# Kernel optimization log

Hardware: AMD Instinct MI355X
Metric: run time of the kernel (lower is better)

## Reference

```python
import jax, jax.numpy as jnp
import numpy as np

N_NODES = 100000


def _gcn_norm(edge_index, n):
    # add self-loops, then symmetric deg^{-1/2} normalization (PyG GCNConv default)
    loop = jnp.arange(n, dtype=edge_index.dtype)
    src = jnp.concatenate([edge_index[0], loop])
    dst = jnp.concatenate([edge_index[1], loop])
    ones = jnp.ones(src.shape[0], dtype=jnp.float32)
    deg = jax.ops.segment_sum(ones, dst, num_segments=n)
    dinv = jnp.where(deg > 0, jax.lax.rsqrt(deg), 0.0)
    norm = dinv[src] * dinv[dst]  # [E + N]
    return src, dst, norm


def _gcn_conv(x, src, dst, norm, W, b, n):
    h = x @ W                                    # [N, out] transform first (out <= in)
    msg = norm[:, None] * h[src]                 # [E+N, out]
    agg = jax.ops.segment_sum(msg, dst, num_segments=n)
    return agg + b


def reference(x, edge_index, W1, b1, W2, b2):
    n = x.shape[0]
    src, dst, norm = _gcn_norm(edge_index, n)
    h = jax.nn.relu(_gcn_conv(x, src, dst, norm, W1, b1, n))
    # dropout is identity in eval mode (training=False)
    h = jax.nn.relu(_gcn_conv(h, src, dst, norm, W2, b2, n))
    return jax.nn.log_softmax(h, axis=1)


def setup_inputs() -> dict:
    key = jax.random.key(0)
    k1, k2, k3, k4 = jax.random.split(key, 4)
    n, e, f, h, c = N_NODES, 1600000, 500, 64, 40
    x = jax.random.normal(k1, (n, f), dtype=jnp.float32)
    edge_index = jax.random.randint(k2, (2, e), 0, n, dtype=jnp.int64)
    W1 = jax.random.normal(k3, (f, h), dtype=jnp.float32) * (1.0 / np.sqrt(f))
    b1 = jnp.zeros((h,), dtype=jnp.float32)
    W2 = jax.random.normal(k4, (h, c), dtype=jnp.float32) * (1.0 / np.sqrt(h))
    b2 = jnp.zeros((c,), dtype=jnp.float32)
    return {"x": x, "edge_index": edge_index, "W1": W1, "b1": b1, "W2": W2, "b2": b2}
```

## Files before the change

### kernel.cpp

```cpp
#include <hip/hip_runtime.h>

#define NN_F 500
#define HID 64
#define NC 40
#define SCAN_T 256
#define SCAN_E 8
#define SCAN_B (SCAN_T * SCAN_E)

typedef short s8v __attribute__((ext_vector_type(8)));
typedef short s4v __attribute__((ext_vector_type(4)));
typedef float f4v __attribute__((ext_vector_type(4)));

struct HL { short h, l; };
__device__ __forceinline__ HL split_bf16(float x) {
    HL r;
    unsigned u = __float_as_uint(x);
    r.h = (short)(u >> 16);
    float hf = __uint_as_float(u & 0xffff0000u);
    r.l = (short)(__float_as_uint(x - hf) >> 16);
    return r;
}

__device__ __forceinline__ unsigned short rne_bf16(float x) {
    unsigned u = __float_as_uint(x);
    return (unsigned short)((u + 0x7fffu + ((u >> 16) & 1u)) >> 16);
}
__device__ __forceinline__ float bf16f(unsigned short v) {
    return __uint_as_float((unsigned)v << 16);
}

__device__ __forceinline__ int load_edge(const void* ei, long long idx, int is64) {
    if (is64) return (int)((const long long*)ei)[idx];
    return ((const int*)ei)[idx];
}

__global__ __launch_bounds__(256) void detect_kernel(const unsigned int* w, int* flag) {
    __shared__ unsigned int red[256];
    unsigned int acc = 0;
    for (int i = threadIdx.x; i < 2048; i += 256) acc |= w[2 * i + 1];
    red[threadIdx.x] = acc;
    __syncthreads();
    for (int s = 128; s > 0; s >>= 1) {
        if (threadIdx.x < s) red[threadIdx.x] |= red[threadIdx.x + s];
        __syncthreads();
    }
    if (threadIdx.x == 0) flag[0] = (red[0] == 0u) ? 1 : 0;
}

__global__ __launch_bounds__(256) void deg_kernel(const void* ei, const int* flag,
                                                  int* deg, int E) {
    int is64 = flag[0];
    long long e = (long long)blockIdx.x * 256 + threadIdx.x;
    if (e < E) {
        int d = load_edge(ei, (long long)E + e, is64);
        atomicAdd(&deg[d], 1);
    }
}

__global__ __launch_bounds__(256) void dinv_kernel(const int* __restrict__ deg,
                                                   float* __restrict__ dinv, int n) {
    int i = blockIdx.x * 256 + threadIdx.x;
    if (i < n) dinv[i] = rsqrtf((float)deg[i] + 1.0f);
}

__global__ __launch_bounds__(SCAN_T) void scan1(const int* __restrict__ deg,
                                                int* __restrict__ off,
                                                int* __restrict__ bsums, int n) {
    __shared__ int lds[SCAN_T];
    int base = blockIdx.x * SCAN_B + threadIdx.x * SCAN_E;
    int v[SCAN_E];
    int local = 0;
#pragma unroll
    for (int k = 0; k < SCAN_E; ++k) {
        v[k] = (base + k < n) ? deg[base + k] : 0;
        local += v[k];
    }
    lds[threadIdx.x] = local;
    __syncthreads();
    for (int o = 1; o < SCAN_T; o <<= 1) {
        int t = (threadIdx.x >= o) ? lds[threadIdx.x - o] : 0;
        __syncthreads();
        lds[threadIdx.x] += t;
        __syncthreads();
    }
    int prefix = lds[threadIdx.x] - local;
    if (threadIdx.x == SCAN_T - 1) bsums[blockIdx.x] = lds[threadIdx.x];
    int run = prefix;
#pragma unroll
    for (int k = 0; k < SCAN_E; ++k) {
        if (base + k < n) { off[base + k] = run; run += v[k]; }
    }
}

__global__ void scan2(int* bsums, int* off, int nb, int n) {
    if (threadIdx.x == 0 && blockIdx.x == 0) {
        int run = 0;
        for (int i = 0; i < nb; ++i) { int t = bsums[i]; bsums[i] = run; run += t; }
        off[n] = run;
    }
}

__global__ __launch_bounds__(SCAN_T) void scan3(int* __restrict__ off,
                                                int* __restrict__ cur,
                                                const int* __restrict__ bsums, int n) {
    int base = blockIdx.x * SCAN_B + threadIdx.x * SCAN_E;
    int add = bsums[blockIdx.x];
#pragma unroll
    for (int k = 0; k < SCAN_E; ++k) {
        int i = base + k;
        if (i < n) { int v = off[i] + add; off[i] = v; cur[i] = v; }
    }
}

__global__ __launch_bounds__(256) void build_kernel(const void* ei, const int* flag,
                                                    const float* __restrict__ dinv,
                                                    int* __restrict__ cur,
                                                    int2* __restrict__ csr, int E) {
    int is64 = flag[0];
    long long e = (long long)blockIdx.x * 256 + threadIdx.x;
    if (e >= E) return;
    int s = load_edge(ei, e, is64);
    int d = load_edge(ei, (long long)E + e, is64);
    int pos = atomicAdd(&cur[d], 1);
    csr[pos] = make_int2(s, (int)__float_as_uint(dinv[s] * dinv[d]));
}

__global__ __launch_bounds__(256) void wprep(const float* __restrict__ W,
                                             short* __restrict__ Wh, short* __restrict__ Wl,
                                             int K, int KP, int Nc, int N) {
    int id = blockIdx.x * 256 + threadIdx.x;
    if (id >= N * KP) return;
    int nn = id / KP, k = id % KP;
    float v = (k < K && nn < Nc) ? W[(long long)k * Nc + nn] : 0.f;
    HL r = split_bf16(v);
    Wh[nn * KP + k] = r.h;
    Wl[nn * KP + k] = r.l;
}

template<int KPAD>
__global__ __launch_bounds__(256) void gemm_mfma(const float* __restrict__ A,
                                                 const short* __restrict__ Wh,
                                                 const short* __restrict__ Wl,
                                                 unsigned short* __restrict__ out,
                                                 int n, int K) {
    __shared__ short Xh[128 * 32], Xl[128 * 32];
    __shared__ short Bh[64 * 32], Bl[64 * 32];
    const int t = threadIdx.x;
    const int row0 = blockIdx.x * 128;
    const int wid = t >> 6, lane = t & 63, q = lane >> 4, nn = lane & 15;

    f4v acc[2][4];
#pragma unroll
    for (int mt = 0; mt < 2; ++mt)
#pragma unroll
        for (int ct = 0; ct < 4; ++ct) acc[mt][ct] = (f4v){0.f, 0.f, 0.f, 0.f};

    for (int k0 = 0; k0 < KPAD; k0 += 32) {
        {
            int bn = t >> 2, kq = t & 3;
            *(s8v*)&Bh[bn * 32 + kq * 8] = *(const s8v*)&Wh[bn * KPAD + k0 + kq * 8];
            *(s8v*)&Bl[bn * 32 + kq * 8] = *(const s8v*)&Wl[bn * KPAD + k0 + kq * 8];
        }
        {
            int kq = t & 7, rbase = t >> 3;
#pragma unroll
            for (int rr = 0; rr < 4; ++rr) {
                int row = rr * 32 + rbase;
                int grow = row0 + row;
                int k = k0 + kq * 4;
                float v0 = 0.f, v1 = 0.f, v2 = 0.f, v3 = 0.f;
                if (grow < n) {
                    if (k + 4 <= K) {
                        float4 v = *(const float4*)&A[(long long)grow * K + k];
                        v0 = v.x; v1 = v.y; v2 = v.z; v3 = v.w;
                    } else {
                        if (k + 0 < K) v0 = A[(long long)grow * K + k + 0];
                        if (k + 1 < K) v1 = A[(long long)grow * K + k + 1];
                        if (k + 2 < K) v2 = A[(long long)grow * K + k + 2];
                        if (k + 3 < K) v3 = A[(long long)grow * K + k + 3];
                    }
                }
                HL r0 = split_bf16(v0), r1 = split_bf16(v1);
                HL r2 = split_bf16(v2), r3 = split_bf16(v3);
                s4v h4, l4;
                h4[0] = r0.h; l4[0] = r0.l;
                h4[1] = r1.h; l4[1] = r1.l;
                h4[2] = r2.h; l4[2] = r2.l;
                h4[3] = r3.h; l4[3] = r3.l;
                *(s4v*)&Xh[row * 32 + kq * 4] = h4;
                *(s4v*)&Xl[row * 32 + kq * 4] = l4;
            }
        }
        __syncthreads();

        const s8v ah0 = *(const s8v*)&Xh[(wid * 32 + nn) * 32 + q * 8];
        const s8v ah1 = *(const s8v*)&Xh[(wid * 32 + 16 + nn) * 32 + q * 8];
        const s8v al0 = *(const s8v*)&Xl[(wid * 32 + nn) * 32 + q * 8];
        const s8v al1 = *(const s8v*)&Xl[(wid * 32 + 16 + nn) * 32 + q * 8];
#pragma unroll
        for (int ct = 0; ct < 4; ++ct) {
            const s8v bh = *(const s8v*)&Bh[(ct * 16 + nn) * 32 + q * 8];
            const s8v bl = *(const s8v*)&Bl[(ct * 16 + nn) * 32 + q * 8];
            acc[0][ct] = __builtin_amdgcn_mfma_f32_16x16x32_bf16(ah0, bh, acc[0][ct], 0, 0, 0);
            acc[0][ct] = __builtin_amdgcn_mfma_f32_16x16x32_bf16(ah0, bl, acc[0][ct], 0, 0, 0);
            acc[0][ct] = __builtin_amdgcn_mfma_f32_16x16x32_bf16(al0, bh, acc[0][ct], 0, 0, 0);
            acc[1][ct] = __builtin_amdgcn_mfma_f32_16x16x32_bf16(ah1, bh, acc[1][ct], 0, 0, 0);
            acc[1][ct] = __builtin_amdgcn_mfma_f32_16x16x32_bf16(ah1, bl, acc[1][ct], 0, 0, 0);
            acc[1][ct] = __builtin_amdgcn_mfma_f32_16x16x32_bf16(al1, bh, acc[1][ct], 0, 0, 0);
        }
        __syncthreads();
    }

#pragma unroll
    for (int mt = 0; mt < 2; ++mt)
#pragma unroll
        for (int ct = 0; ct < 4; ++ct)
#pragma unroll
            for (int r = 0; r < 4; ++r) {
                int row = row0 + wid * 32 + mt * 16 + q * 4 + r;
                if (row < n) out[(long long)row * 64 + ct * 16 + nn] = rne_bf16(acc[mt][ct][r]);
            }
}

__global__ __launch_bounds__(256) void gather_l1(const int2* __restrict__ csr,
                                                 const int* __restrict__ off,
                                                 const unsigned short* __restrict__ h,
                                                 const float* __restrict__ dinv,
                                                 const float* __restrict__ b,
                                                 float* __restrict__ agg, int n) {
    const int lane = threadIdx.x & 63;
    const int node = __builtin_amdgcn_readfirstlane(blockIdx.x * 4 + (threadIdx.x >> 6));
    if (node >= n) return;
    int start = off[node], end = off[node + 1];
    float dv = dinv[node];
    float acc = dv * dv * bf16f(h[(long long)node * 64 + lane]);
    int j = start;
    for (; j + 4 <= end; j += 4) {
        int2 e0 = csr[j + 0], e1 = csr[j + 1], e2 = csr[j + 2], e3 = csr[j + 3];
        float f0 = bf16f(h[(long long)e0.x * 64 + lane]);
        float f1 = bf16f(h[(long long)e1.x * 64 + lane]);
        float f2 = bf16f(h[(long long)e2.x * 64 + lane]);
        float f3 = bf16f(h[(long long)e3.x * 64 + lane]);
        acc = fmaf(__uint_as_float((unsigned)e0.y), f0, acc);
        acc = fmaf(__uint_as_float((unsigned)e1.y), f1, acc);
        acc = fmaf(__uint_as_float((unsigned)e2.y), f2, acc);
        acc = fmaf(__uint_as_float((unsigned)e3.y), f3, acc);
    }
    for (; j < end; ++j) {
        int2 e = csr[j];
        acc = fmaf(__uint_as_float((unsigned)e.y), bf16f(h[(long long)e.x * 64 + lane]), acc);
    }
    float v = acc + b[lane];
    agg[(long long)node * 64 + lane] = v > 0.f ? v : 0.f;
}

__global__ __launch_bounds__(256) void gather_l2(const int2* __restrict__ csr,
                                                 const int* __restrict__ off,
                                                 const unsigned short* __restrict__ h,
                                                 const float* __restrict__ dinv,
                                                 const float* __restrict__ b,
                                                 float* __restrict__ out, int n) {
    const int lane = threadIdx.x & 63;
    const int node = __builtin_amdgcn_readfirstlane(blockIdx.x * 4 + (threadIdx.x >> 6));
    if (node >= n) return;
    int start = off[node], end = off[node + 1];
    float dv = dinv[node];
    const int act = (lane < NC) ? 1 : 0;
    float acc = act ? dv * dv * bf16f(h[(long long)node * 64 + lane]) : 0.f;
    int j = start;
    for (; j + 4 <= end; j += 4) {
        int2 e0 = csr[j + 0], e1 = csr[j + 1], e2 = csr[j + 2], e3 = csr[j + 3];
        if (act) {
            float f0 = bf16f(h[(long long)e0.x * 64 + lane]);
            float f1 = bf16f(h[(long long)e1.x * 64 + lane]);
            float f2 = bf16f(h[(long long)e2.x * 64 + lane]);
            float f3 = bf16f(h[(long long)e3.x * 64 + lane]);
            acc = fmaf(__uint_as_float((unsigned)e0.y), f0, acc);
            acc = fmaf(__uint_as_float((unsigned)e1.y), f1, acc);
            acc = fmaf(__uint_as_float((unsigned)e2.y), f2, acc);
            acc = fmaf(__uint_as_float((unsigned)e3.y), f3, acc);
        }
    }
    for (; j < end; ++j) {
        int2 e = csr[j];
        if (act) acc = fmaf(__uint_as_float((unsigned)e.y),
                            bf16f(h[(long long)e.x * 64 + lane]), acc);
    }
    float tv;
    if (act) {
        tv = acc + b[lane];
        tv = tv > 0.f ? tv : 0.f;
    } else {
        tv = -1e30f;
    }
    float m = tv;
#pragma unroll
    for (int o = 32; o > 0; o >>= 1) m = fmaxf(m, __shfl_xor(m, o));
    float ex = act ? expf(tv - m) : 0.f;
    float ssum = ex;
#pragma unroll
    for (int o = 32; o > 0; o >>= 1) ssum += __shfl_xor(ssum, o);
    if (act) out[(long long)node * NC + lane] = tv - m - logf(ssum);
}

static inline char* align256(char* p) {
    return (char*)(((uintptr_t)p + 255) & ~(uintptr_t)255);
}

extern "C" void kernel_launch(void* const* d_in, const int* in_sizes, int n_in,
                              void* d_out, int out_size, void* d_ws, size_t ws_size,
                              hipStream_t stream) {
    const float* x  = (const float*)d_in[0];
    const void*  ei = d_in[1];
    const float* W1 = (const float*)d_in[2];
    const float* b1 = (const float*)d_in[3];
    const float* W2 = (const float*)d_in[4];
    const float* b2 = (const float*)d_in[5];
    float* out = (float*)d_out;
    const int n = in_sizes[0] / NN_F;
    const int E = in_sizes[1] / 2;
    const int nScanBlocks = (n + SCAN_B - 1) / SCAN_B;

    char* p = (char*)d_ws;
    int* flag = (int*)p;                 p = align256(p + 16 * sizeof(int));
    int* deg  = (int*)p;                 p = align256(p + (size_t)n * sizeof(int));
    int* off  = (int*)p;                 p = align256(p + (size_t)(n + 1) * sizeof(int));
    int* cur  = (int*)p;                 p = align256(p + (size_t)n * sizeof(int));
    int* bsums = (int*)p;                p = align256(p + 256 * sizeof(int));
    float* dinv = (float*)p;             p = align256(p + (size_t)n * sizeof(float));
    int2* csr = (int2*)p;                p = align256(p + (size_t)E * sizeof(int2));
    short* Wt1h = (short*)p;             p = align256(p + (size_t)64 * 512 * sizeof(short));
    short* Wt1l = (short*)p;             p = align256(p + (size_t)64 * 512 * sizeof(short));
    short* Wt2h = (short*)p;             p = align256(p + (size_t)64 * 64 * sizeof(short));
    short* Wt2l = (short*)p;             p = align256(p + (size_t)64 * 64 * sizeof(short));
    unsigned short* h1 = (unsigned short*)p; p = align256(p + (size_t)n * 64 * sizeof(unsigned short));
    float* agg1 = (float*)p;             p = align256(p + (size_t)n * 64 * sizeof(float));
    unsigned short* h2 = h1;

    (void)hipMemsetAsync(deg, 0, (size_t)n * sizeof(int), stream);
    detect_kernel<<<1, 256, 0, stream>>>((const unsigned int*)ei, flag);
    deg_kernel<<<(E + 255) / 256, 256, 0, stream>>>(ei, flag, deg, E);
    dinv_kernel<<<(n + 255) / 256, 256, 0, stream>>>(deg, dinv, n);

    scan1<<<nScanBlocks, SCAN_T, 0, stream>>>(deg, off, bsums, n);
    scan2<<<1, 64, 0, stream>>>(bsums, off, nScanBlocks, n);
    scan3<<<nScanBlocks, SCAN_T, 0, stream>>>(off, cur, bsums, n);
    build_kernel<<<(E + 255) / 256, 256, 0, stream>>>(ei, flag, dinv, cur, csr, E);

    wprep<<<(64 * 512 + 255) / 256, 256, 0, stream>>>(W1, Wt1h, Wt1l, NN_F, 512, HID, 64);
    wprep<<<(64 * 64 + 255) / 256, 256, 0, stream>>>(W2, Wt2h, Wt2l, HID, 64, NC, 64);

    const int gBlocks = (n + 127) / 128;
    gemm_mfma<512><<<gBlocks, 256, 0, stream>>>(x, Wt1h, Wt1l, h1, n, NN_F);
    gather_l1<<<(n + 3) / 4, 256, 0, stream>>>(csr, off, h1, dinv, b1, agg1, n);

    gemm_mfma<64><<<gBlocks, 256, 0, stream>>>(agg1, Wt2h, Wt2l, h2, n, HID);
    gather_l2<<<(n + 3) / 4, 256, 0, stream>>>(csr, off, h2, dinv, b2, out, n);
}
```

Before: 607.6 us.

## Use single bf16 MFMA GEMM and vectorized 4-edge-parallel gathers

Drops the split-bf16 (hi/lo) three-MFMA emulation of fp32 GEMM in favour of a single round-to-nearest bf16 product, which halves the shared-memory staging and cuts the MFMA count to a third. The gather kernels are restructured so each wavefront handles 4 edges at a time, with 16 lanes each loading 4 bf16 features as a uint2, followed by a cross-group shuffle reduction. Bias, ReLU and log-softmax are vectorized over float4. The GEMM loses some accuracy because the input and weight products are no longer split into hi/lo parts.

Measured after the change: 593.3 us. 1.02x faster.

```diff
diff --git a/kernel.cpp b/kernel.cpp
--- a/kernel.cpp
+++ b/kernel.cpp
@@ -11,22 +11,15 @@
 typedef short s4v __attribute__((ext_vector_type(4)));
 typedef float f4v __attribute__((ext_vector_type(4)));
 
-struct HL { short h, l; };
-__device__ __forceinline__ HL split_bf16(float x) {
-    HL r;
-    unsigned u = __float_as_uint(x);
-    r.h = (short)(u >> 16);
-    float hf = __uint_as_float(u & 0xffff0000u);
-    r.l = (short)(__float_as_uint(x - hf) >> 16);
-    return r;
-}
-
 __device__ __forceinline__ unsigned short rne_bf16(float x) {
     unsigned u = __float_as_uint(x);
     return (unsigned short)((u + 0x7fffu + ((u >> 16) & 1u)) >> 16);
 }
-__device__ __forceinline__ float bf16f(unsigned short v) {
-    return __uint_as_float((unsigned)v << 16);
+__device__ __forceinline__ float bf16_lo(unsigned v) {
+    return __uint_as_float(v << 16);
+}
+__device__ __forceinline__ float bf16_hi(unsigned v) {
+    return __uint_as_float(v & 0xffff0000u);
 }
 
 __device__ __forceinline__ int load_edge(const void* ei, long long idx, int is64) {
@@ -126,25 +119,22 @@
 }
 
 __global__ __launch_bounds__(256) void wprep(const float* __restrict__ W,
-                                             short* __restrict__ Wh, short* __restrict__ Wl,
+                                             unsigned short* __restrict__ Wh,
                                              int K, int KP, int Nc, int N) {
     int id = blockIdx.x * 256 + threadIdx.x;
     if (id >= N * KP) return;
     int nn = id / KP, k = id % KP;
     float v = (k < K && nn < Nc) ? W[(long long)k * Nc + nn] : 0.f;
-    HL r = split_bf16(v);
-    Wh[nn * KP + k] = r.h;
-    Wl[nn * KP + k] = r.l;
+    Wh[nn * KP + k] = rne_bf16(v);
 }
 
 template<int KPAD>
 __global__ __launch_bounds__(256) void gemm_mfma(const float* __restrict__ A,
-                                                 const short* __restrict__ Wh,
-                                                 const short* __restrict__ Wl,
+                                                 const unsigned short* __restrict__ Wh,
                                                  unsigned short* __restrict__ out,
                                                  int n, int K) {
-    __shared__ short Xh[128 * 32], Xl[128 * 32];
-    __shared__ short Bh[64 * 32], Bl[64 * 32];
+    __shared__ unsigned short Xh[128 * 32];
+    __shared__ unsigned short Bh[64 * 32];
     const int t = threadIdx.x;
     const int row0 = blockIdx.x * 128;
     const int wid = t >> 6, lane = t & 63, q = lane >> 4, nn = lane & 15;
@@ -159,7 +149,6 @@
         {
             int bn = t >> 2, kq = t & 3;
             *(s8v*)&Bh[bn * 32 + kq * 8] = *(const s8v*)&Wh[bn * KPAD + k0 + kq * 8];
-            *(s8v*)&Bl[bn * 32 + kq * 8] = *(const s8v*)&Wl[bn * KPAD + k0 + kq * 8];
         }
         {
             int kq = t & 7, rbase = t >> 3;
@@ -180,33 +169,23 @@
                         if (k + 3 < K) v3 = A[(long long)grow * K + k + 3];
                     }
                 }
-                HL r0 = split_bf16(v0), r1 = split_bf16(v1);
-                HL r2 = split_bf16(v2), r3 = split_bf16(v3);
-                s4v h4, l4;
-                h4[0] = r0.h; l4[0] = r0.l;
-                h4[1] = r1.h; l4[1] = r1.l;
-                h4[2] = r2.h; l4[2] = r2.l;
-                h4[3] = r3.h; l4[3] = r3.l;
+                s4v h4;
+                h4[0] = (short)rne_bf16(v0);
+                h4[1] = (short)rne_bf16(v1);
+                h4[2] = (short)rne_bf16(v2);
+                h4[3] = (short)rne_bf16(v3);
                 *(s4v*)&Xh[row * 32 + kq * 4] = h4;
-                *(s4v*)&Xl[row * 32 + kq * 4] = l4;
             }
         }
         __syncthreads();
 
         const s8v ah0 = *(const s8v*)&Xh[(wid * 32 + nn) * 32 + q * 8];
         const s8v ah1 = *(const s8v*)&Xh[(wid * 32 + 16 + nn) * 32 + q * 8];
-        const s8v al0 = *(const s8v*)&Xl[(wid * 32 + nn) * 32 + q * 8];
-        const s8v al1 = *(const s8v*)&Xl[(wid * 32 + 16 + nn) * 32 + q * 8];
 #pragma unroll
         for (int ct = 0; ct < 4; ++ct) {
             const s8v bh = *(const s8v*)&Bh[(ct * 16 + nn) * 32 + q * 8];
-            const s8v bl = *(const s8v*)&Bl[(ct * 16 + nn) * 32 + q * 8];
             acc[0][ct] = __builtin_amdgcn_mfma_f32_16x16x32_bf16(ah0, bh, acc[0][ct], 0, 0, 0);
-            acc[0][ct] = __builtin_amdgcn_mfma_f32_16x16x32_bf16(ah0, bl, acc[0][ct], 0, 0, 0);
-            acc[0][ct] = __builtin_amdgcn_mfma_f32_16x16x32_bf16(al0, bh, acc[0][ct], 0, 0, 0);
             acc[1][ct] = __builtin_amdgcn_mfma_f32_16x16x32_bf16(ah1, bh, acc[1][ct], 0, 0, 0);
-            acc[1][ct] = __builtin_amdgcn_mfma_f32_16x16x32_bf16(ah1, bl, acc[1][ct], 0, 0, 0);
-            acc[1][ct] = __builtin_amdgcn_mfma_f32_16x16x32_bf16(al1, bh, acc[1][ct], 0, 0, 0);
         }
         __syncthreads();
     }
@@ -229,29 +208,58 @@
                                                  const float* __restrict__ b,
                                                  float* __restrict__ agg, int n) {
     const int lane = threadIdx.x & 63;
+    const int g = lane >> 4, fp = lane & 15;
     const int node = __builtin_amdgcn_readfirstlane(blockIdx.x * 4 + (threadIdx.x >> 6));
     if (node >= n) return;
-    int start = off[node], end = off[node + 1];
+    const int start = off[node], end = off[node + 1];
+    f4v acc = (f4v){0.f, 0.f, 0.f, 0.f};
+    int j = start;
+    for (; j + 8 <= end; j += 8) {
+        int2 ea = csr[j + g];
+        int2 eb = csr[j + 4 + g];
+        uint2 ha = *(const uint2*)(h + (long long)ea.x * 64 + fp * 4);
+        uint2 hb = *(const uint2*)(h + (long long)eb.x * 64 + fp * 4);
+        float wa = __uint_as_float((unsigned)ea.y);
+        float wb = __uint_as_float((unsigned)eb.y);
+        acc[0] = fmaf(wa, bf16_lo(ha.x), acc[0]);
+        acc[1] = fmaf(wa, bf16_hi(ha.x), acc[1]);
+        acc[2] = fmaf(wa, bf16_lo(ha.y), acc[2]);
+        acc[3] = fmaf(wa, bf16_hi(ha.y), acc[3]);
+        acc[0] = fmaf(wb, bf16_lo(hb.x), acc[0]);
+        acc[1] = fmaf(wb, bf16_hi(hb.x), acc[1]);
+        acc[2] = fmaf(wb, bf16_lo(hb.y), acc[2]);
+        acc[3] = fmaf(wb, bf16_hi(hb.y), acc[3]);
+    }
+    for (; j < end; j += 4) {
+        int jj = j + g;
+        int2 e = csr[jj < end ? jj : end - 1];
+        float w = (jj < end) ? __uint_as_float((unsigned)e.y) : 0.f;
+        uint2 hv = *(const uint2*)(h + (long long)e.x * 64 + fp * 4);
+        acc[0] = fmaf(w, bf16_lo(hv.x), acc[0]);
+        acc[1] = fmaf(w, bf16_hi(hv.x), acc[1]);
+        acc[2] = fmaf(w, bf16_lo(hv.y), acc[2]);
+        acc[3] = fmaf(w, bf16_hi(hv.y), acc[3]);
+    }
+#pragma unroll
+    for (int k = 0; k < 4; ++k) {
+        acc[k] += __shfl_xor(acc[k], 16);
+        acc[k] += __shfl_xor(acc[k], 32);
+    }
     float dv = dinv[node];
-    float acc = dv * dv * bf16f(h[(long long)node * 64 + lane]);
-    int j = start;
-    for (; j + 4 <= end; j += 4) {
-        int2 e0 = csr[j + 0], e1 = csr[j + 1], e2 = csr[j + 2], e3 = csr[j + 3];
-        float f0 = bf16f(h[(long long)e0.x * 64 + lane]);
-        float f1 = bf16f(h[(long long)e1.x * 64 + lane]);
-        float f2 = bf16f(h[(long long)e2.x * 64 + lane]);
-        float f3 = bf16f(h[(long long)e3.x * 64 + lane]);
-        acc = fmaf(__uint_as_float((unsigned)e0.y), f0, acc);
-        acc = fmaf(__uint_as_float((unsigned)e1.y), f1, acc);
-        acc = fmaf(__uint_as_float((unsigned)e2.y), f2, acc);
-        acc = fmaf(__uint_as_float((unsigned)e3.y), f3, acc);
-    }
-    for (; j < end; ++j) {
-        int2 e = csr[j];
-        acc = fmaf(__uint_as_float((unsigned)e.y), bf16f(h[(long long)e.x * 64 + lane]), acc);
-    }
-    float v = acc + b[lane];
-    agg[(long long)node * 64 + lane] = v > 0.f ? v : 0.f;
+    uint2 hn = *(const uint2*)(h + (long long)node * 64 + fp * 4);
+    acc[0] = fmaf(dv * dv, bf16_lo(hn.x), acc[0]);
+    acc[1] = fmaf(dv * dv, bf16_hi(hn.x), acc[1]);
+    acc[2] = fmaf(dv * dv, bf16_lo(hn.y), acc[2]);
+    acc[3] = fmaf(dv * dv, bf16_hi(hn.y), acc[3]);
+    float4 b4 = ((const float4*)b)[fp];
+    if (g == 0) {
+        float4 v;
+        v.x = acc[0] + b4.x; v.x = v.x > 0.f ? v.x : 0.f;
+        v.y = acc[1] + b4.y; v.y = v.y > 0.f ? v.y : 0.f;
+        v.z = acc[2] + b4.z; v.z = v.z > 0.f ? v.z : 0.f;
+        v.w = acc[3] + b4.w; v.w = v.w > 0.f ? v.w : 0.f;
+        ((float4*)(agg + (long long)node * 64))[fp] = v;
+    }
 }
 
 __global__ __launch_bounds__(256) void gather_l2(const int2* __restrict__ csr,
@@ -261,46 +269,71 @@
                                                  const float* __restrict__ b,
                                                  float* __restrict__ out, int n) {
     const int lane = threadIdx.x & 63;
+    const int g = lane >> 4, fp = lane & 15;
     const int node = __builtin_amdgcn_readfirstlane(blockIdx.x * 4 + (threadIdx.x >> 6));
     if (node >= n) return;
-    int start = off[node], end = off[node + 1];
+    const int start = off[node], end = off[node + 1];
+    f4v acc = (f4v){0.f, 0.f, 0.f, 0.f};
+    int j = start;
+    for (; j + 8 <= end; j += 8) {
+        int2 ea = csr[j + g];
+        int2 eb = csr[j + 4 + g];
+        uint2 ha = *(const uint2*)(h + (long long)ea.x * 64 + fp * 4);
+        uint2 hb = *(const uint2*)(h + (long long)eb.x * 64 + fp * 4);
+        float wa = __uint_as_float((unsigned)ea.y);
+        float wb = __uint_as_float((unsigned)eb.y);
+        acc[0] = fmaf(wa, bf16_lo(ha.x), acc[0]);
+        acc[1] = fmaf(wa, bf16_hi(ha.x), acc[1]);
+        acc[2] = fmaf(wa, bf16_lo(ha.y), acc[2]);
+        acc[3] = fmaf(wa, bf16_hi(ha.y), acc[3]);
+        acc[0] = fmaf(wb, bf16_lo(hb.x), acc[0]);
+        acc[1] = fmaf(wb, bf16_hi(hb.x), acc[1]);
+        acc[2] = fmaf(wb, bf16_lo(hb.y), acc[2]);
+        acc[3] = fmaf(wb, bf16_hi(hb.y), acc[3]);
+    }
+    for (; j < end; j += 4) {
+        int jj = j + g;
+        int2 e = csr[jj < end ? jj : end - 1];
+        float w = (jj < end) ? __uint_as_float((unsigned)e.y) : 0.f;
+        uint2 hv = *(const uint2*)(h + (long long)e.x * 64 + fp * 4);
+        acc[0] = fmaf(w, bf16_lo(hv.x), acc[0]);
+        acc[1] = fmaf(w, bf16_hi(hv.x), acc[1]);
+        acc[2] = fmaf(w, bf16_lo(hv.y), acc[2]);
+        acc[3] = fmaf(w, bf16_hi(hv.y), acc[3]);
+    }
+#pragma unroll
+    for (int k = 0; k < 4; ++k) {
+        acc[k] += __shfl_xor(acc[k], 16);
+        acc[k] += __shfl_xor(acc[k], 32);
+    }
     float dv = dinv[node];
-    const int act = (lane < NC) ? 1 : 0;
-    float acc = act ? dv * dv * bf16f(h[(long long)node * 64 + lane]) : 0.f;
-    int j = start;
-    for (; j + 4 <= end; j += 4) {
-        int2 e0 = csr[j + 0], e1 = csr[j + 1], e2 = csr[j + 2], e3 = csr[j + 3];
-        if (act) {
-            float f0 = bf16f(h[(long long)e0.x * 64 + lane]);
-            float f1 = bf16f(h[(long long)e1.x * 64 + lane]);
-            float f2 = bf16f(h[(long long)e2.x * 64 + lane]);
-            float f3 = bf16f(h[(long long)e3.x * 64 + lane]);
-            acc = fmaf(__uint_as_float((unsigned)e0.y), f0, acc);
-            acc = fmaf(__uint_as_float((unsigned)e1.y), f1, acc);
-            acc = fmaf(__uint_as_float((unsigned)e2.y), f2, acc);
-            acc = fmaf(__uint_as_float((unsigned)e3.y), f3, acc);
-        }
-    }
-    for (; j < end; ++j) {
-        int2 e = csr[j];
-        if (act) acc = fmaf(__uint_as_float((unsigned)e.y),
-                            bf16f(h[(long long)e.x * 64 + lane]), acc);
-    }
-    float tv;
-    if (act) {
-        tv = acc + b[lane];
-        tv = tv > 0.f ? tv : 0.f;
+    uint2 hn = *(const uint2*)(h + (long long)node * 64 + fp * 4);
+    acc[0] = fmaf(dv * dv, bf16_lo(hn.x), acc[0]);
+    acc[1] = fmaf(dv * dv, bf16_hi(hn.x), acc[1]);
+    acc[2] = fmaf(dv * dv, bf16_lo(hn.y), acc[2]);
+    acc[3] = fmaf(dv * dv, bf16_hi(hn.y), acc[3]);
+    float t0, t1, t2, t3;
+    if (fp < 10) {
+        float4 b4 = ((const float4*)b)[fp];
+        t0 = acc[0] + b4.x; t0 = t0 > 0.f ? t0 : 0.f;
+        t1 = acc[1] + b4.y; t1 = t1 > 0.f ? t1 : 0.f;
+        t2 = acc[2] + b4.z; t2 = t2 > 0.f ? t2 : 0.f;
+        t3 = acc[3] + b4.w; t3 = t3 > 0.f ? t3 : 0.f;
     } else {
-        tv = -1e30f;
-    }
-    float m = tv;
-#pragma unroll
-    for (int o = 32; o > 0; o >>= 1) m = fmaxf(m, __shfl_xor(m, o));
-    float ex = act ? expf(tv - m) : 0.f;
-    float ssum = ex;
-#pragma unroll
-    for (int o = 32; o > 0; o >>= 1) ssum += __shfl_xor(ssum, o);
-    if (act) out[(long long)node * NC + lane] = tv - m - logf(ssum);
+        t0 = t1 = t2 = t3 = -1e30f;
+    }
+    float m = fmaxf(fmaxf(t0, t1), fmaxf(t2, t3));
+#pragma unroll
+    for (int o = 1; o < 16; o <<= 1) m = fmaxf(m, __shfl_xor(m, o));
+    float ssum = 0.f;
+    if (fp < 10) ssum = expf(t0 - m) + expf(t1 - m) + expf(t2 - m) + expf(t3 - m);
+#pragma unroll
+    for (int o = 1; o < 16; o <<= 1) ssum += __shfl_xor(ssum, o);
+    if (g == 0 && fp < 10) {
+        float ls = m + logf(ssum);
+        float4 v = make_float4(t0 - ls, t1 - ls, t2 - ls, t3 - ls);
+        ((float4*)(out + (long long)node * NC))[fp] = v;
+    }
 }
 
 static inline char* align256(char* p) {
@@ -329,10 +362,8 @@
     int* bsums = (int*)p;                p = align256(p + 256 * sizeof(int));
     float* dinv = (float*)p;             p = align256(p + (size_t)n * sizeof(float));
     int2* csr = (int2*)p;                p = align256(p + (size_t)E * sizeof(int2));
-    short* Wt1h = (short*)p;             p = align256(p + (size_t)64 * 512 * sizeof(short));
-    short* Wt1l = (short*)p;             p = align256(p + (size_t)64 * 512 * sizeof(short));
-    short* Wt2h = (short*)p;             p = align256(p + (size_t)64 * 64 * sizeof(short));
-    short* Wt2l = (short*)p;             p = align256(p + (size_t)64 * 64 * sizeof(short));
+    unsigned short* Wt1 = (unsigned short*)p; p = align256(p + (size_t)64 * 512 * sizeof(short));
+    unsigned short* Wt2 = (unsigned short*)p; p = align256(p + (size_t)64 * 64 * sizeof(short));
     unsigned short* h1 = (unsigned short*)p; p = align256(p + (size_t)n * 64 * sizeof(unsigned short));
     float* agg1 = (float*)p;             p = align256(p + (size_t)n * 64 * sizeof(float));
     unsigned short* h2 = h1;
@@ -347,13 +378,13 @@
     scan3<<<nScanBlocks, SCAN_T, 0, stream>>>(off, cur, bsums, n);
     build_kernel<<<(E + 255) / 256, 256, 0, stream>>>(ei, flag, dinv, cur, csr, E);
 
-    wprep<<<(64 * 512 + 255) / 256, 256, 0, stream>>>(W1, Wt1h, Wt1l, NN_F, 512, HID, 64);
-    wprep<<<(64 * 64 + 255) / 256, 256, 0, stream>>>(W2, Wt2h, Wt2l, HID, 64, NC, 64);
+    wprep<<<(64 * 512 + 255) / 256, 256, 0, stream>>>(W1, Wt1, NN_F, 512, HID, 64);
+    wprep<<<(64 * 64 + 255) / 256, 256, 0, stream>>>(W2, Wt2, HID, 64, NC, 64);
 
     const int gBlocks = (n + 127) / 128;
-    gemm_mfma<512><<<gBlocks, 256, 0, stream>>>(x, Wt1h, Wt1l, h1, n, NN_F);
+    gemm_mfma<512><<<gBlocks, 256, 0, stream>>>(x, Wt1, h1, n, NN_F);
     gather_l1<<<(n + 3) / 4, 256, 0, stream>>>(csr, off, h1, dinv, b1, agg1, n);
 
-    gemm_mfma<64><<<gBlocks, 256, 0, stream>>>(agg1, Wt2h, Wt2l, h2, n, HID);
+    gemm_mfma<64><<<gBlocks, 256, 0, stream>>>(agg1, Wt2, h2, n, HID);
     gather_l2<<<(n + 3) / 4, 256, 0, stream>>>(csr, off, h2, dinv, b2, out, n);
 }
```
